# Optimization experiments

Measured on AMD Instinct MI355X. Metric: run time of the kernel, lower is better.

## Reference

```python
import jax, jax.numpy as jnp
import numpy as np
import math

H = 12  # config['n_heads']

def _ln(x, w, b, eps=1e-5):
    mu = x.mean(-1, keepdims=True)
    var = ((x - mu) ** 2).mean(-1, keepdims=True)
    return (x - mu) / jnp.sqrt(var + eps) * w + b

def setup_inputs() -> dict:
    key = jax.random.key(0)
    B, L, D, R = 2, 1024, 768, 128
    d_head = D // H
    ks = jax.random.split(key, 6)
    s = 0.02
    return {
        "x": jax.random.normal(ks[0], (B, L, D), jnp.float32),
        "Wqkv": jax.random.normal(ks[1], (D, 3 * D), jnp.float32) * s,
        "bqkv": jnp.zeros((3 * D,), jnp.float32),
        "Wb1": jax.random.normal(ks[2], (D, R), jnp.float32) * s,
        "Wb2": jax.random.normal(ks[3], (R, H * 5), jnp.float32) * s,
        "temperature": jnp.ones((1,), jnp.float32) * 0.5,
        "Wproj": jax.random.normal(ks[4], (D, D), jnp.float32) * s,
        "bproj": jnp.zeros((D,), jnp.float32),
        "ln_w": jnp.ones((D,), jnp.float32),
        "ln_b": jnp.zeros((D,), jnp.float32),
        "mn_w": jnp.ones((d_head,), jnp.float32),
        "mn_b": jnp.zeros((d_head,), jnp.float32),
    }

def reference(x, Wqkv, bqkv, Wb1, Wb2, temperature, Wproj, bproj, ln_w, ln_b, mn_w, mn_b):
    B, L, D = x.shape
    d = D // H
    x_norm = _ln(x, ln_w, ln_b)
    qkv = x_norm @ Wqkv + bqkv
    q, k, v = jnp.split(qkv, 3, axis=-1)
    # bottleneck gating operates on raw x (not x_norm), matching the source
    params = (jax.nn.silu(x @ Wb1) @ Wb2).reshape(B, L, H, 5)
    sem_amp = jax.nn.sigmoid(params[..., 0])
    sem_phase = jnp.tanh(params[..., 1]) * math.pi
    ctx_amp = jax.nn.sigmoid(params[..., 2])
    ctx_phase = jnp.tanh(params[..., 3]) * math.pi
    # decay_rate = 0.1 + 0.89*sigmoid(params[...,4]) is computed in the source
    # but never used in the final output path, so it is omitted here.
    temp = jnp.clip(temperature, 0.1, 2.0)  # shape (1,), broadcasts
    interference = jnp.tanh(sem_amp * ctx_amp * jnp.cos(sem_phase - ctx_phase)) * temp
    gate = jax.nn.sigmoid(interference)  # [B,L,H]
    q_f = (jax.nn.elu(q) + 1.0).reshape(B, L, H, d)
    k_f = (jax.nn.elu(k) + 1.0).reshape(B, L, H, d)
    v_f = v.reshape(B, L, H, d)
    # gated KV outer products and causal prefix-sum (linear attention state)
    kv_gated = jnp.einsum('blhd,blhe->blhde', k_f, v_f) * (1.0 + gate)[..., None, None]
    kv_states = jnp.cumsum(kv_gated, axis=1)       # [B,L,H,d,d]
    z_states = jnp.cumsum(k_f, axis=1)             # [B,L,H,d]
    out_num = jnp.einsum('blhd,blhde->blhe', q_f, kv_states)
    den = jnp.sum(q_f * z_states, axis=-1, keepdims=True) + 1e-6
    out = _ln(out_num / den, mn_w, mn_b)           # LayerNorm over d_head
    attn_out = out.reshape(B, L, D)
    return (attn_out @ Wproj + bproj, gate)
```

## Files before the change

kernel.cpp:

```cpp
#include <hip/hip_runtime.h>
#include <hip/hip_bf16.h>
#include <math.h>

constexpr int Bc = 2, Lc = 1024, Dc = 768, Hc = 12, dh = 64, Rc = 128;
constexpr int BL = Bc * Lc;
constexpr int TD = 3 * Dc;
constexpr int CH = 64;
constexpr int NC = Lc / CH;
constexpr int BH = Bc * Hc;

typedef __attribute__((ext_vector_type(8))) short bf16x8;
typedef __attribute__((ext_vector_type(4))) float f32x4;

__device__ __forceinline__ float bf2f(short u) {
    union { float f; unsigned int i; } c;
    c.i = ((unsigned int)(unsigned short)u) << 16;
    return c.f;
}
__device__ __forceinline__ short f2b(float f) {
    __hip_bfloat16 h = __float2bfloat16(f);
    return *reinterpret_cast<short*>(&h);
}

#define GLOAD_LDS16(gp, lp)                                                        \
    __builtin_amdgcn_global_load_lds(                                              \
        (const __attribute__((address_space(1))) void*)(gp),                       \
        (__attribute__((address_space(3))) void*)(lp), 16, 0, 0)

__device__ __forceinline__ void do_transpose(const float* __restrict__ W,
                                             __hip_bfloat16* __restrict__ WT,
                                             int K, int N, int bx, int by,
                                             int tid, float* t) {
    int k0 = by * 32, n0 = bx * 32;
    int r = tid >> 5, c = tid & 31;
#pragma unroll
    for (int i = 0; i < 4; i++)
        t[(r + i * 8) * 33 + c] = W[(size_t)(k0 + r + i * 8) * N + n0 + c];
    __syncthreads();
#pragma unroll
    for (int i = 0; i < 4; i++)
        WT[(size_t)(n0 + r + i * 8) * K + k0 + c] = __float2bfloat16(t[c * 33 + r + i * 8]);
}

constexpr int NT1 = (TD / 32) * (Dc / 32);
constexpr int NT2 = (Dc / 32) * (Dc / 32);
constexpr int NT3 = (Rc / 32) * (Dc / 32);
constexpr int NPREP = NT1 + NT2 + NT3 + BL;

__global__ __launch_bounds__(256)
void prep_kernel(const float* __restrict__ x, const float* __restrict__ ln_w,
                 const float* __restrict__ ln_b,
                 const float* __restrict__ Wqkv, const float* __restrict__ Wproj,
                 const float* __restrict__ Wb1,
                 __hip_bfloat16* __restrict__ xnb, __hip_bfloat16* __restrict__ xb,
                 __hip_bfloat16* __restrict__ WqkvT, __hip_bfloat16* __restrict__ WprojT,
                 __hip_bfloat16* __restrict__ Wb1T) {
    __shared__ float shm[32 * 33];
    int bid = blockIdx.x, tid = threadIdx.x;
    if (bid < NT1) { do_transpose(Wqkv, WqkvT, Dc, TD, bid % 72, bid / 72, tid, shm); return; }
    bid -= NT1;
    if (bid < NT2) { do_transpose(Wproj, WprojT, Dc, Dc, bid % 24, bid / 24, tid, shm); return; }
    bid -= NT2;
    if (bid < NT3) { do_transpose(Wb1, Wb1T, Dc, Rc, bid % 4, bid / 4, tid, shm); return; }
    bid -= NT3;
    int row = bid;
    const float* xr = x + (size_t)row * Dc;
    __hip_bfloat16* yr = xnb + (size_t)row * Dc;
    __hip_bfloat16* xbr = xb + (size_t)row * Dc;
    float v[3];
    float s = 0.f;
#pragma unroll
    for (int i = 0; i < 3; i++) { v[i] = xr[tid + i * 256]; s += v[i]; }
    shm[tid] = s; __syncthreads();
    for (int off = 128; off > 0; off >>= 1) {
        if (tid < off) shm[tid] += shm[tid + off];
        __syncthreads();
    }
    float mu = shm[0] / (float)Dc;
    __syncthreads();
    float s2 = 0.f;
#pragma unroll
    for (int i = 0; i < 3; i++) { float d = v[i] - mu; s2 += d * d; }
    shm[tid] = s2; __syncthreads();
    for (int off = 128; off > 0; off >>= 1) {
        if (tid < off) shm[tid] += shm[tid + off];
        __syncthreads();
    }
    float rstd = rsqrtf(shm[0] / (float)Dc + 1e-5f);
#pragma unroll
    for (int i = 0; i < 3; i++) {
        int c = tid + i * 256;
        yr[c] = __float2bfloat16((v[i] - mu) * rstd * ln_w[c] + ln_b[c]);
        xbr[c] = __float2bfloat16(v[i]);
    }
}

constexpr int NQB = (BL / 128) * (TD / 64);
constexpr int NFAT = NQB + (BL / 128) * 2;
__global__ __launch_bounds__(256)
void fat_gemm_kernel(const __hip_bfloat16* __restrict__ A1,
                     const __hip_bfloat16* __restrict__ B1,
                     const float* __restrict__ bias1,
                     __hip_bfloat16* __restrict__ C1,
                     const __hip_bfloat16* __restrict__ A2,
                     const __hip_bfloat16* __restrict__ B2,
                     float* __restrict__ C2) {
    __shared__ short lds[2][128 * 64 + 64 * 64];
    int bid = blockIdx.x;
    bid = (bid & 7) * (NFAT / 8) + (bid >> 3);
    bool isq = bid < NQB;
    int bx, by, N;
    const __hip_bfloat16 *A, *BT;
    if (isq) { bx = bid % 36; by = bid / 36; A = A1; BT = B1; N = TD; }
    else     { int b2 = bid - NQB; bx = b2 % 2; by = b2 / 2; A = A2; BT = B2; N = Rc; }
    const int K = Dc;

    int tid = threadIdx.x;
    int wave = tid >> 6, lane = tid & 63;
    int l16 = lane & 15, l4 = lane >> 4;
    int m0 = by * 128, n0 = bx * 64;

    int r_in = lane >> 3;
    int s_src = (lane & 7) ^ r_in;
    const __hip_bfloat16* gsrcA = A  + (size_t)(m0 + wave * 32 + r_in) * K + s_src * 8;
    const __hip_bfloat16* gsrcB = BT + (size_t)(n0 + wave * 16 + r_in) * K + s_src * 8;

    int wr = (wave >> 1) * 64, wc = (wave & 1) * 32;
    int xs = l16 & 7;

    f32x4 acc[4][2];
#pragma unroll
    for (int i = 0; i < 4; i++)
#pragma unroll
        for (int j = 0; j < 2; j++) acc[i][j] = f32x4{0.f, 0.f, 0.f, 0.f};

    auto stage = [&](int buf, int kt) {
        short* lbA = &lds[buf][(wave * 32) * 64];
        short* lbB = &lds[buf][128 * 64 + (wave * 16) * 64];
        const __hip_bfloat16* gA = gsrcA + kt * 64;
        const __hip_bfloat16* gB = gsrcB + kt * 64;
#pragma unroll
        for (int i = 0; i < 4; i++)
            GLOAD_LDS16(gA + (size_t)i * 8 * K, lbA + i * 8 * 64);
#pragma unroll
        for (int i = 0; i < 2; i++)
            GLOAD_LDS16(gB + (size_t)i * 8 * K, lbB + i * 8 * 64);
    };
    auto compute = [&](int buf) {
        const short* As = &lds[buf][0];
        const short* Bs = &lds[buf][128 * 64];
#pragma unroll
        for (int kk = 0; kk < 2; kk++) {
            bf16x8 af[4], bfr[2];
            int slot = (kk * 4 + l4) ^ xs;
#pragma unroll
            for (int f = 0; f < 4; f++)
                af[f] = *reinterpret_cast<const bf16x8*>(
                    &As[(wr + f * 16 + l16) * 64 + slot * 8]);
#pragma unroll
            for (int f = 0; f < 2; f++)
                bfr[f] = *reinterpret_cast<const bf16x8*>(
                    &Bs[(wc + f * 16 + l16) * 64 + slot * 8]);
#pragma unroll
            for (int i = 0; i < 4; i++)
#pragma unroll
                for (int j = 0; j < 2; j++)
                    acc[i][j] = __builtin_amdgcn_mfma_f32_16x16x32_bf16(
                        af[i], bfr[j], acc[i][j], 0, 0, 0);
        }
    };

    int NT = K / 64;
    int cur = 0;
    stage(0, 0);
    __syncthreads();
    for (int t = 0; t < NT; t++) {
        if (t + 1 < NT) stage(cur ^ 1, t + 1);
        compute(cur);
        if (t + 1 < NT) { __syncthreads(); cur ^= 1; }
    }

    int crow = l4 * 4;
#pragma unroll
    for (int i = 0; i < 4; i++) {
#pragma unroll
        for (int j = 0; j < 2; j++) {
            int col = n0 + wc + j * 16 + l16;
            float bb = isq ? bias1[col] : 0.f;
#pragma unroll
            for (int r = 0; r < 4; r++) {
                int rowm = m0 + wr + i * 16 + crow + r;
                float v = acc[i][j][r] + bb;
                if (isq) {
                    C1[(size_t)rowm * N + col] = __float2bfloat16(v);
                } else {
                    v = v / (1.f + expf(-v));
                    C2[(size_t)rowm * N + col] = v;
                }
            }
        }
    }
}

__global__ __launch_bounds__(256)
void gemm64_kernel(const __hip_bfloat16* __restrict__ A,
                   const __hip_bfloat16* __restrict__ BT,
                   const float* __restrict__ bias,
                   float* __restrict__ C, int M, int N, int K, int nbx) {
    __shared__ short lds[2][128 * 64];
    int nwg = gridDim.x;
    int bid = blockIdx.x;
    if ((nwg & 7) == 0) bid = (bid & 7) * (nwg >> 3) + (bid >> 3);
    int m0 = (bid / nbx) * 64, n0 = (bid % nbx) * 64;

    int tid = threadIdx.x;
    int wave = tid >> 6, lane = tid & 63;
    int l16 = lane & 15, l4 = lane >> 4;

    int r_in = lane >> 3;
    int s_src = (lane & 7) ^ r_in;
    const __hip_bfloat16* gsrc = (wave < 2)
        ? A  + (size_t)(m0 + wave * 32 + r_in) * K + s_src * 8
        : BT + (size_t)(n0 + (wave - 2) * 32 + r_in) * K + s_src * 8;

    int wr = (wave >> 1) * 32, wc = (wave & 1) * 32;
    int xs = l16 & 7;

    f32x4 acc[2][2];
#pragma unroll
    for (int i = 0; i < 2; i++)
#pragma unroll
        for (int j = 0; j < 2; j++) acc[i][j] = f32x4{0.f, 0.f, 0.f, 0.f};

    auto stage = [&](int buf, int kt) {
        const __hip_bfloat16* g = gsrc + kt * 64;
        short* lb = &lds[buf][wave * 32 * 64];
#pragma unroll
        for (int i = 0; i < 4; i++)
            GLOAD_LDS16(g + (size_t)i * 8 * K, lb + i * 8 * 64);
    };
    auto compute = [&](int buf) {
        const short* As = &lds[buf][0];
        const short* Bs = &lds[buf][64 * 64];
#pragma unroll
        for (int kk = 0; kk < 2; kk++) {
            bf16x8 af[2], bfr[2];
            int slot = (kk * 4 + l4) ^ xs;
#pragma unroll
            for (int f = 0; f < 2; f++) {
                af[f]  = *reinterpret_cast<const bf16x8*>(
                    &As[(wr + f * 16 + l16) * 64 + slot * 8]);
                bfr[f] = *reinterpret_cast<const bf16x8*>(
                    &Bs[(wc + f * 16 + l16) * 64 + slot * 8]);
            }
#pragma unroll
            for (int i = 0; i < 2; i++)
#pragma unroll
                for (int j = 0; j < 2; j++)
                    acc[i][j] = __builtin_amdgcn_mfma_f32_16x16x32_bf16(
                        af[i], bfr[j], acc[i][j], 0, 0, 0);
        }
    };

    int NT = K / 64;
    int cur = 0;
    stage(0, 0);
    __syncthreads();
    for (int t = 0; t < NT; t++) {
        if (t + 1 < NT) stage(cur ^ 1, t + 1);
        compute(cur);
        if (t + 1 < NT) { __syncthreads(); cur ^= 1; }
    }

    int crow = l4 * 4;
#pragma unroll
    for (int i = 0; i < 2; i++) {
#pragma unroll
        for (int j = 0; j < 2; j++) {
            int col = n0 + wc + j * 16 + l16;
            float bb = bias[col];
#pragma unroll
            for (int r = 0; r < 4; r++) {
                int rowm = m0 + wr + i * 16 + crow + r;
                C[(size_t)rowm * N + col] = acc[i][j][r] + bb;
            }
        }
    }
}

constexpr int LQ = 72;
__global__ __launch_bounds__(256)
void phaseA_kernel(const __hip_bfloat16* __restrict__ qkv, const float* __restrict__ tbuf,
                   const float* __restrict__ Wb2, const float* __restrict__ temperature,
                   float* __restrict__ gate_out,
                   float* __restrict__ SU, float* __restrict__ zc) {
    int bid = blockIdx.x;
    int bh = bid >> 4, c = bid & 15;
    int b = bh / Hc, h = bh % Hc;
    int tok0 = b * Lc + c * CH;
    __shared__ short KsT[64 * LQ];
    __shared__ short VT[80 * LQ];
    __shared__ float w2s[5 * 128];
    __shared__ float ogs[64];
    int tid = threadIdx.x;
    int wave = tid >> 6, lane = tid & 63;
    int l16 = lane & 15, l4 = lane >> 4;

    for (int i = tid; i < 640; i += 256) {
        int cc = i >> 7, r = i & 127;
        w2s[i] = Wb2[r * (Hc * 5) + h * 5 + cc];
    }
    bf16x8 k8[2], v8[2];
#pragma unroll
    for (int i = 0; i < 2; i++) {
        int c8 = tid + i * 256;
        int tt = c8 >> 3, d8 = (c8 & 7) * 8;
        size_t rowoff = (size_t)(tok0 + tt) * TD + h * dh;
        k8[i] = *reinterpret_cast<const bf16x8*>(qkv + rowoff + Dc + d8);
        v8[i] = *reinterpret_cast<const bf16x8*>(qkv + rowoff + 2 * Dc + d8);
    }
    for (int i = tid; i < 16 * LQ; i += 256) VT[64 * LQ + i] = 0;
    if (tid < 64) VT[64 * LQ + tid] = f2b(1.0f);
    __syncthreads();

    {
        int tt = tid >> 2, sub = tid & 3;
        const float* tr = tbuf + (size_t)(tok0 + tt) * Rc + sub * 32;
        float p[5] = {};
        for (int r4 = 0; r4 < 32; r4 += 4) {
            float4 tv = *reinterpret_cast<const float4*>(tr + r4);
#pragma unroll
            for (int cc = 0; cc < 5; cc++) {
                float4 w4 = *reinterpret_cast<const float4*>(&w2s[cc * 128 + sub * 32 + r4]);
                p[cc] = fmaf(tv.x, w4.x, fmaf(tv.y, w4.y,
                        fmaf(tv.z, w4.z, fmaf(tv.w, w4.w, p[cc]))));
            }
        }
#pragma unroll
        for (int cc = 0; cc < 5; cc++) {
            p[cc] += __shfl_xor(p[cc], 1, 64);
            p[cc] += __shfl_xor(p[cc], 2, 64);
        }
        if (sub == 0) {
            const float PI = 3.14159265358979323846f;
            float sem_amp = 1.f / (1.f + expf(-p[0]));
            float sem_phase = tanhf(p[1]) * PI;
            float ctx_amp = 1.f / (1.f + expf(-p[2]));
            float ctx_phase = tanhf(p[3]) * PI;
            float temp = fminf(fmaxf(temperature[0], 0.1f), 2.0f);
            float inter = tanhf(sem_amp * ctx_amp * cosf(sem_phase - ctx_phase)) * temp;
            float g = 1.f / (1.f + expf(-inter));
            gate_out[(size_t)(tok0 + tt) * Hc + h] = g;
            ogs[tt] = 1.f + g;
        }
    }
    __syncthreads();

#pragma unroll
    for (int i = 0; i < 2; i++) {
        int c8 = tid + i * 256;
        int tt = c8 >> 3, d8 = (c8 & 7) * 8;
        float gv = ogs[tt];
#pragma unroll
        for (int j = 0; j < 8; j++) {
            float kv = bf2f(k8[i][j]);
            KsT[(d8 + j) * LQ + tt] = f2b(kv > 0.f ? kv + 1.f : expf(kv));
            VT[(d8 + j) * LQ + tt]  = f2b(bf2f(v8[i][j]) * gv);
        }
    }
    __syncthreads();

    const short* arow = &KsT[(wave * 16 + l16) * LQ];
    f32x4 acc[5];
#pragma unroll
    for (int j = 0; j < 5; j++) acc[j] = f32x4{0.f, 0.f, 0.f, 0.f};
#pragma unroll
    for (int kk = 0; kk < 2; kk++) {
        bf16x8 af = *reinterpret_cast<const bf16x8*>(&arow[kk * 32 + l4 * 8]);
#pragma unroll
        for (int j = 0; j < 5; j++) {
            bf16x8 bfv = *reinterpret_cast<const bf16x8*>(
                &VT[(j * 16 + l16) * LQ + kk * 32 + l4 * 8]);
            acc[j] = __builtin_amdgcn_mfma_f32_16x16x32_bf16(af, bfv, acc[j], 0, 0, 0);
        }
    }
    int dbase = wave * 16 + l4 * 4;
    float* SUo = SU + (size_t)bid * 4096;
#pragma unroll
    for (int j = 0; j < 4; j++) {
        int e = j * 16 + l16;
#pragma unroll
        for (int r = 0; r < 4; r++)
            SUo[e * 64 + dbase + r] = acc[j][r];
    }
    if (l16 == 0) {
#pragma unroll
        for (int r = 0; r < 4; r++)
            zc[bid * 64 + dbase + r] = acc[4][r];
    }
}

__global__ __launch_bounds__(256)
void prefix_kernel(float* __restrict__ SU, float* __restrict__ zc) {
    int gid = blockIdx.x * 256 + threadIdx.x;
    if (gid < BH * 4096) {
        int bh = gid >> 12, i = gid & 4095;
        float* S = SU + (size_t)bh * NC * 4096 + i;
        float r[NC];
#pragma unroll
        for (int cc = 0; cc < NC; cc++) r[cc] = S[cc * 4096];
        float run = 0.f;
#pragma unroll
        for (int cc = 0; cc < NC; cc++) { float tv = r[cc]; S[cc * 4096] = run; run += tv; }
    } else {
        int g2 = gid - BH * 4096;
        if (g2 < BH * 64) {
            int bh = g2 >> 6, i = g2 & 63;
            float* z = zc + (size_t)bh * NC * 64 + i;
            float r[NC];
#pragma unroll
            for (int cc = 0; cc < NC; cc++) r[cc] = z[cc * 64];
            float run = 0.f;
#pragma unroll
            for (int cc = 0; cc < NC; cc++) { float tv = r[cc]; z[cc * 64] = run; run += tv; }
        }
    }
}

constexpr int LB = 136;
__global__ __launch_bounds__(256)
void phaseC_kernel(const __hip_bfloat16* __restrict__ qkv, const float* __restrict__ gate,
                   const float* __restrict__ SU, const float* __restrict__ zc,
                   const float* __restrict__ mn_w, const float* __restrict__ mn_b,
                   __hip_bfloat16* __restrict__ attn) {
    int bid = blockIdx.x;
    int bh = bid >> 4;
    int b = bh / Hc, h = bh % Hc;
    int tok0 = b * Lc + (bid & 15) * CH;
    __shared__ short Qs[64 * LQ];
    __shared__ short Ks[64 * LQ];
    __shared__ short Ps[64 * LQ];
    __shared__ short Bst[80 * LB];
    int tid = threadIdx.x;
    int wave = tid >> 6, lane = tid & 63;
    int l16 = lane & 15, l4 = lane >> 4;

    const float* SUp = SU + (size_t)bid * 4096;
    const float* zcp = zc + (size_t)bid * 64;

#pragma unroll
    for (int i = 0; i < 2; i++) {
        int c8 = tid + i * 256;
        int tt = c8 >> 3, d8 = (c8 & 7) * 8;
        size_t rowoff = (size_t)(tok0 + tt) * TD + h * dh;
        bf16x8 q8 = *reinterpret_cast<const bf16x8*>(qkv + rowoff + d8);
        bf16x8 k8 = *reinterpret_cast<const bf16x8*>(qkv + rowoff + Dc + d8);
        bf16x8 v8 = *reinterpret_cast<const bf16x8*>(qkv + rowoff + 2 * Dc + d8);
        float gv = 1.f + gate[(size_t)(tok0 + tt) * Hc + h];
        short qo[8], ko[8];
#pragma unroll
        for (int j = 0; j < 8; j++) {
            float qv = bf2f(q8[j]);
            qo[j] = f2b(qv > 0.f ? qv + 1.f : expf(qv));
            float kv = bf2f(k8[j]);
            ko[j] = f2b(kv > 0.f ? kv + 1.f : expf(kv));
            Bst[(d8 + j) * LB + tt] = f2b(bf2f(v8[j]) * gv);
        }
        *reinterpret_cast<bf16x8*>(&Qs[tt * LQ + d8]) = *reinterpret_cast<bf16x8*>(qo);
        *reinterpret_cast<bf16x8*>(&Ks[tt * LQ + d8]) = *reinterpret_cast<bf16x8*>(ko);
        float4 sa = *reinterpret_cast<const float4*>(SUp + tt * 64 + d8);
        float4 sb = *reinterpret_cast<const float4*>(SUp + tt * 64 + d8 + 4);
        short so[8] = { f2b(sa.x), f2b(sa.y), f2b(sa.z), f2b(sa.w),
                        f2b(sb.x), f2b(sb.y), f2b(sb.z), f2b(sb.w) };
        *reinterpret_cast<bf16x8*>(&Bst[tt * LB + 64 + d8]) = *reinterpret_cast<bf16x8*>(so);
    }
    if (tid < 64) {
        Bst[64 * LB + tid] = f2b(1.0f);
        Bst[64 * LB + 64 + tid] = f2b(zcp[tid]);
    } else {
        for (int i2 = tid - 64; i2 < 15 * LB; i2 += 192) Bst[65 * LB + i2] = 0;
    }
    __syncthreads();

    const short* arow = &Qs[(wave * 16 + l16) * LQ];
    f32x4 accp[4];
#pragma unroll
    for (int j = 0; j < 4; j++) accp[j] = f32x4{0.f, 0.f, 0.f, 0.f};
#pragma unroll
    for (int kk = 0; kk < 2; kk++) {
        bf16x8 af = *reinterpret_cast<const bf16x8*>(&arow[kk * 32 + l4 * 8]);
#pragma unroll
        for (int j = 0; j < 4; j++) {
            bf16x8 bfv = *reinterpret_cast<const bf16x8*>(
                &Ks[(j * 16 + l16) * LQ + kk * 32 + l4 * 8]);
            accp[j] = __builtin_amdgcn_mfma_f32_16x16x32_bf16(af, bfv, accp[j], 0, 0, 0);
        }
    }
#pragma unroll
    for (int j = 0; j < 4; j++) {
#pragma unroll
        for (int r = 0; r < 4; r++) {
            int l = wave * 16 + l4 * 4 + r;
            int t = j * 16 + l16;
            float pv = (t <= l) ? accp[j][r] : 0.f;
            Ps[l * LQ + t] = f2b(pv);
        }
    }
    __syncthreads();

    const short* prow = &Ps[(wave * 16 + l16) * LQ];
    f32x4 acc[5];
#pragma unroll
    for (int j = 0; j < 5; j++) acc[j] = f32x4{0.f, 0.f, 0.f, 0.f};
#pragma unroll
    for (int kk = 0; kk < 4; kk++) {
        bf16x8 af = (kk < 2)
            ? *reinterpret_cast<const bf16x8*>(&prow[kk * 32 + l4 * 8])
            : *reinterpret_cast<const bf16x8*>(&arow[(kk - 2) * 32 + l4 * 8]);
#pragma unroll
        for (int j = 0; j < 5; j++) {
            bf16x8 bfv = *reinterpret_cast<const bf16x8*>(
                &Bst[(j * 16 + l16) * LB + kk * 32 + l4 * 8]);
            acc[j] = __builtin_amdgcn_mfma_f32_16x16x32_bf16(af, bfv, acc[j], 0, 0, 0);
        }
    }

#pragma unroll
    for (int r = 0; r < 4; r++) {
        float den = __shfl(acc[4][r], l4 * 16) + 1e-6f;
        float inv = 1.f / den;
        float v0 = acc[0][r] * inv, v1 = acc[1][r] * inv;
        float v2 = acc[2][r] * inv, v3 = acc[3][r] * inv;
        float s1 = v0 + v1 + v2 + v3;
        float s2 = v0 * v0 + v1 * v1 + v2 * v2 + v3 * v3;
#pragma unroll
        for (int m = 1; m < 16; m <<= 1) {
            s1 += __shfl_xor(s1, m, 64);
            s2 += __shfl_xor(s2, m, 64);
        }
        float mu = s1 * (1.f / 64.f);
        float rstd = rsqrtf(s2 * (1.f / 64.f) - mu * mu + 1e-5f);
        int l = wave * 16 + l4 * 4 + r;
        __hip_bfloat16* orow = attn + (size_t)(tok0 + l) * Dc + h * dh;
        float vj[4] = {v0, v1, v2, v3};
#pragma unroll
        for (int j = 0; j < 4; j++) {
            int e = j * 16 + l16;
            orow[e] = __float2bfloat16((vj[j] - mu) * rstd * mn_w[e] + mn_b[e]);
        }
    }
}

extern "C" void kernel_launch(void* const* d_in, const int* in_sizes, int n_in,
                              void* d_out, int out_size, void* d_ws, size_t ws_size,
                              hipStream_t stream) {
    const float* x     = (const float*)d_in[0];
    const float* Wqkv  = (const float*)d_in[1];
    const float* bqkv  = (const float*)d_in[2];
    const float* Wb1   = (const float*)d_in[3];
    const float* Wb2   = (const float*)d_in[4];
    const float* temp  = (const float*)d_in[5];
    const float* Wproj = (const float*)d_in[6];
    const float* bproj = (const float*)d_in[7];
    const float* ln_w  = (const float*)d_in[8];
    const float* ln_b  = (const float*)d_in[9];
    const float* mn_w  = (const float*)d_in[10];
    const float* mn_b  = (const float*)d_in[11];

    float* out0 = (float*)d_out;
    float* gate = out0 + (size_t)BL * Dc;

    float* ws   = (float*)d_ws;
    float* tbuf = ws;
    float* SU   = tbuf + (size_t)BL * Rc;
    float* zc   = SU + (size_t)BH * NC * 4096;
    __hip_bfloat16* bfr = (__hip_bfloat16*)(zc + (size_t)BH * NC * 64);
    __hip_bfloat16* qkvb   = bfr;
    __hip_bfloat16* xnb    = qkvb + (size_t)BL * TD;
    __hip_bfloat16* xb     = xnb + (size_t)BL * Dc;
    __hip_bfloat16* attnb  = xb + (size_t)BL * Dc;
    __hip_bfloat16* WqkvT  = attnb + (size_t)BL * Dc;
    __hip_bfloat16* WprojT = WqkvT + (size_t)TD * Dc;
    __hip_bfloat16* Wb1T   = WprojT + (size_t)Dc * Dc;

    prep_kernel<<<NPREP, 256, 0, stream>>>(x, ln_w, ln_b, Wqkv, Wproj, Wb1,
                                           xnb, xb, WqkvT, WprojT, Wb1T);
    fat_gemm_kernel<<<NFAT, 256, 0, stream>>>(xnb, WqkvT, bqkv, qkvb, xb, Wb1T, tbuf);
    phaseA_kernel<<<BH * NC, 256, 0, stream>>>(qkvb, tbuf, Wb2, temp, gate, SU, zc);
    prefix_kernel<<<(BH * 4096 + BH * 64 + 255) / 256, 256, 0, stream>>>(SU, zc);
    phaseC_kernel<<<BH * NC, 256, 0, stream>>>(qkvb, gate, SU, zc, mn_w, mn_b, attnb);
    gemm64_kernel<<<(BL / 64) * (Dc / 64), 256, 0, stream>>>(
        attnb, WprojT, bproj, out0, BL, Dc, Dc, Dc / 64);
}
```

Before: 58.68 us.

## Fuse phaseA, prefix, phaseC and projection GEMM into persistent kernel with grid barriers

Merges the four post-QKV kernels into one launch of 384 blocks that synchronise through a software grid barrier built on atomics. Each block keeps its Q, K and gated V tiles in shared memory from phase A into phase C, so they are not reloaded from global memory. This removes three launch gaps and the tail idling between kernels. In exchange it adds the cost of the atomic spin barriers and a memset per call, and it depends on all 384 blocks being resident at once; launch bounds of 256 threads with 2 blocks per CU are set to allow that.

```diff
diff --git a/kernel.cpp b/kernel.cpp
--- a/kernel.cpp
+++ b/kernel.cpp
@@ -8,6 +8,7 @@
 constexpr int CH = 64;
 constexpr int NC = Lc / CH;
 constexpr int BH = Bc * Hc;
+constexpr int NMEGA = BH * NC;
 
 typedef __attribute__((ext_vector_type(8))) short bf16x8;
 typedef __attribute__((ext_vector_type(4))) float f32x4;
@@ -26,6 +27,26 @@
     __builtin_amdgcn_global_load_lds(                                              \
         (const __attribute__((address_space(1))) void*)(gp),                       \
         (__attribute__((address_space(3))) void*)(lp), 16, 0, 0)
+
+__device__ __forceinline__ void grid_barrier(unsigned* bar, int idx, unsigned nb) {
+    __syncthreads();
+    if (threadIdx.x == 0) {
+        unsigned* cnt   = bar + idx * 16;
+        unsigned* sense = bar + idx * 16 + 8;
+        __threadfence();
+        unsigned old = atomicAdd(sense, 0u);
+        if (atomicAdd(cnt, 1u) == nb - 1) {
+            atomicExch(cnt, 0u);
+            __threadfence();
+            atomicAdd(sense, 1u);
+        } else {
+            while (atomicAdd(sense, 0u) == old)
+                __builtin_amdgcn_s_sleep(8);
+        }
+        __threadfence();
+    }
+    __syncthreads();
+}
 
 __device__ __forceinline__ void do_transpose(const float* __restrict__ W,
                                              __hip_bfloat16* __restrict__ WT,
@@ -202,124 +223,48 @@
     }
 }
 
-__global__ __launch_bounds__(256)
-void gemm64_kernel(const __hip_bfloat16* __restrict__ A,
-                   const __hip_bfloat16* __restrict__ BT,
-                   const float* __restrict__ bias,
-                   float* __restrict__ C, int M, int N, int K, int nbx) {
-    __shared__ short lds[2][128 * 64];
-    int nwg = gridDim.x;
+constexpr int LQ = 72;
+__global__ __launch_bounds__(256, 2)
+void mega_kernel(const __hip_bfloat16* __restrict__ qkv, const float* __restrict__ tbuf,
+                 const float* __restrict__ Wb2, const float* __restrict__ temperature,
+                 float* __restrict__ gate_out, float* __restrict__ SU, float* __restrict__ zc,
+                 const float* __restrict__ mn_w, const float* __restrict__ mn_b,
+                 __hip_bfloat16* __restrict__ attn,
+                 const __hip_bfloat16* __restrict__ WprojT, const float* __restrict__ bproj,
+                 float* __restrict__ out0, unsigned* __restrict__ bar) {
+    alignas(16) __shared__ char pool[50688];
+    short* VT   = (short*)pool;
+    short* KsT  = (short*)(pool + 11520);
+    short* Qs   = (short*)(pool + 20736);
+    short* KsRM = (short*)(pool + 29952);
+    float* w2s  = (float*)(pool + 39168);
+    float* ogs  = (float*)(pool + 41728);
+    short* BstS = (short*)(pool + 39168);
+
     int bid = blockIdx.x;
-    if ((nwg & 7) == 0) bid = (bid & 7) * (nwg >> 3) + (bid >> 3);
-    int m0 = (bid / nbx) * 64, n0 = (bid % nbx) * 64;
-
     int tid = threadIdx.x;
     int wave = tid >> 6, lane = tid & 63;
     int l16 = lane & 15, l4 = lane >> 4;
 
-    int r_in = lane >> 3;
-    int s_src = (lane & 7) ^ r_in;
-    const __hip_bfloat16* gsrc = (wave < 2)
-        ? A  + (size_t)(m0 + wave * 32 + r_in) * K + s_src * 8
-        : BT + (size_t)(n0 + (wave - 2) * 32 + r_in) * K + s_src * 8;
-
-    int wr = (wave >> 1) * 32, wc = (wave & 1) * 32;
-    int xs = l16 & 7;
-
-    f32x4 acc[2][2];
-#pragma unroll
-    for (int i = 0; i < 2; i++)
-#pragma unroll
-        for (int j = 0; j < 2; j++) acc[i][j] = f32x4{0.f, 0.f, 0.f, 0.f};
-
-    auto stage = [&](int buf, int kt) {
-        const __hip_bfloat16* g = gsrc + kt * 64;
-        short* lb = &lds[buf][wave * 32 * 64];
-#pragma unroll
-        for (int i = 0; i < 4; i++)
-            GLOAD_LDS16(g + (size_t)i * 8 * K, lb + i * 8 * 64);
-    };
-    auto compute = [&](int buf) {
-        const short* As = &lds[buf][0];
-        const short* Bs = &lds[buf][64 * 64];
-#pragma unroll
-        for (int kk = 0; kk < 2; kk++) {
-            bf16x8 af[2], bfr[2];
-            int slot = (kk * 4 + l4) ^ xs;
-#pragma unroll
-            for (int f = 0; f < 2; f++) {
-                af[f]  = *reinterpret_cast<const bf16x8*>(
-                    &As[(wr + f * 16 + l16) * 64 + slot * 8]);
-                bfr[f] = *reinterpret_cast<const bf16x8*>(
-                    &Bs[(wc + f * 16 + l16) * 64 + slot * 8]);
-            }
-#pragma unroll
-            for (int i = 0; i < 2; i++)
-#pragma unroll
-                for (int j = 0; j < 2; j++)
-                    acc[i][j] = __builtin_amdgcn_mfma_f32_16x16x32_bf16(
-                        af[i], bfr[j], acc[i][j], 0, 0, 0);
-        }
-    };
-
-    int NT = K / 64;
-    int cur = 0;
-    stage(0, 0);
-    __syncthreads();
-    for (int t = 0; t < NT; t++) {
-        if (t + 1 < NT) stage(cur ^ 1, t + 1);
-        compute(cur);
-        if (t + 1 < NT) { __syncthreads(); cur ^= 1; }
-    }
-
-    int crow = l4 * 4;
-#pragma unroll
-    for (int i = 0; i < 2; i++) {
-#pragma unroll
-        for (int j = 0; j < 2; j++) {
-            int col = n0 + wc + j * 16 + l16;
-            float bb = bias[col];
-#pragma unroll
-            for (int r = 0; r < 4; r++) {
-                int rowm = m0 + wr + i * 16 + crow + r;
-                C[(size_t)rowm * N + col] = acc[i][j][r] + bb;
-            }
-        }
-    }
-}
-
-constexpr int LQ = 72;
-__global__ __launch_bounds__(256)
-void phaseA_kernel(const __hip_bfloat16* __restrict__ qkv, const float* __restrict__ tbuf,
-                   const float* __restrict__ Wb2, const float* __restrict__ temperature,
-                   float* __restrict__ gate_out,
-                   float* __restrict__ SU, float* __restrict__ zc) {
-    int bid = blockIdx.x;
     int bh = bid >> 4, c = bid & 15;
     int b = bh / Hc, h = bh % Hc;
     int tok0 = b * Lc + c * CH;
-    __shared__ short KsT[64 * LQ];
-    __shared__ short VT[80 * LQ];
-    __shared__ float w2s[5 * 128];
-    __shared__ float ogs[64];
-    int tid = threadIdx.x;
-    int wave = tid >> 6, lane = tid & 63;
-    int l16 = lane & 15, l4 = lane >> 4;
 
     for (int i = tid; i < 640; i += 256) {
         int cc = i >> 7, r = i & 127;
         w2s[i] = Wb2[r * (Hc * 5) + h * 5 + cc];
     }
-    bf16x8 k8[2], v8[2];
+    bf16x8 q8[2], k8[2], v8[2];
 #pragma unroll
     for (int i = 0; i < 2; i++) {
         int c8 = tid + i * 256;
         int tt = c8 >> 3, d8 = (c8 & 7) * 8;
         size_t rowoff = (size_t)(tok0 + tt) * TD + h * dh;
+        q8[i] = *reinterpret_cast<const bf16x8*>(qkv + rowoff + d8);
         k8[i] = *reinterpret_cast<const bf16x8*>(qkv + rowoff + Dc + d8);
         v8[i] = *reinterpret_cast<const bf16x8*>(qkv + rowoff + 2 * Dc + d8);
     }
-    for (int i = tid; i < 16 * LQ; i += 256) VT[64 * LQ + i] = 0;
+    for (int i = tid; i < 15 * LQ; i += 256) VT[65 * LQ + i] = 0;
     if (tid < 64) VT[64 * LQ + tid] = f2b(1.0f);
     __syncthreads();
 
@@ -361,192 +306,238 @@
         int c8 = tid + i * 256;
         int tt = c8 >> 3, d8 = (c8 & 7) * 8;
         float gv = ogs[tt];
+        short qo[8], ko[8];
 #pragma unroll
         for (int j = 0; j < 8; j++) {
+            float qv = bf2f(q8[i][j]);
+            qo[j] = f2b(qv > 0.f ? qv + 1.f : expf(qv));
             float kv = bf2f(k8[i][j]);
-            KsT[(d8 + j) * LQ + tt] = f2b(kv > 0.f ? kv + 1.f : expf(kv));
+            ko[j] = f2b(kv > 0.f ? kv + 1.f : expf(kv));
+            KsT[(d8 + j) * LQ + tt] = ko[j];
             VT[(d8 + j) * LQ + tt]  = f2b(bf2f(v8[i][j]) * gv);
         }
-    }
-    __syncthreads();
-
-    const short* arow = &KsT[(wave * 16 + l16) * LQ];
-    f32x4 acc[5];
-#pragma unroll
-    for (int j = 0; j < 5; j++) acc[j] = f32x4{0.f, 0.f, 0.f, 0.f};
-#pragma unroll
-    for (int kk = 0; kk < 2; kk++) {
-        bf16x8 af = *reinterpret_cast<const bf16x8*>(&arow[kk * 32 + l4 * 8]);
-#pragma unroll
-        for (int j = 0; j < 5; j++) {
-            bf16x8 bfv = *reinterpret_cast<const bf16x8*>(
-                &VT[(j * 16 + l16) * LQ + kk * 32 + l4 * 8]);
-            acc[j] = __builtin_amdgcn_mfma_f32_16x16x32_bf16(af, bfv, acc[j], 0, 0, 0);
-        }
-    }
-    int dbase = wave * 16 + l4 * 4;
-    float* SUo = SU + (size_t)bid * 4096;
-#pragma unroll
-    for (int j = 0; j < 4; j++) {
-        int e = j * 16 + l16;
-#pragma unroll
-        for (int r = 0; r < 4; r++)
-            SUo[e * 64 + dbase + r] = acc[j][r];
-    }
-    if (l16 == 0) {
-#pragma unroll
-        for (int r = 0; r < 4; r++)
-            zc[bid * 64 + dbase + r] = acc[4][r];
-    }
-}
-
-__global__ __launch_bounds__(256)
-void prefix_kernel(float* __restrict__ SU, float* __restrict__ zc) {
-    int gid = blockIdx.x * 256 + threadIdx.x;
-    if (gid < BH * 4096) {
-        int bh = gid >> 12, i = gid & 4095;
-        float* S = SU + (size_t)bh * NC * 4096 + i;
+        *reinterpret_cast<bf16x8*>(&Qs[tt * LQ + d8])   = *reinterpret_cast<bf16x8*>(qo);
+        *reinterpret_cast<bf16x8*>(&KsRM[tt * LQ + d8]) = *reinterpret_cast<bf16x8*>(ko);
+    }
+    __syncthreads();
+
+    {
+        const short* arow = &KsT[(wave * 16 + l16) * LQ];
+        f32x4 acc[5];
+#pragma unroll
+        for (int j = 0; j < 5; j++) acc[j] = f32x4{0.f, 0.f, 0.f, 0.f};
+#pragma unroll
+        for (int kk = 0; kk < 2; kk++) {
+            bf16x8 af = *reinterpret_cast<const bf16x8*>(&arow[kk * 32 + l4 * 8]);
+#pragma unroll
+            for (int j = 0; j < 5; j++) {
+                bf16x8 bfv = *reinterpret_cast<const bf16x8*>(
+                    &VT[(j * 16 + l16) * LQ + kk * 32 + l4 * 8]);
+                acc[j] = __builtin_amdgcn_mfma_f32_16x16x32_bf16(af, bfv, acc[j], 0, 0, 0);
+            }
+        }
+        int dbase = wave * 16 + l4 * 4;
+        float* SUo = SU + (size_t)bid * 4096;
+#pragma unroll
+        for (int j = 0; j < 4; j++) {
+            int e = j * 16 + l16;
+#pragma unroll
+            for (int r = 0; r < 4; r++)
+                SUo[e * 64 + dbase + r] = acc[j][r];
+        }
+        if (l16 == 0) {
+#pragma unroll
+            for (int r = 0; r < 4; r++)
+                zc[bid * 64 + dbase + r] = acc[4][r];
+        }
+    }
+    grid_barrier(bar, 0, NMEGA);
+
+    {
+        int gid = bid * 256 + tid;
+        int pbh = gid >> 12, i = gid & 4095;
+        float* S = SU + (size_t)pbh * NC * 4096 + i;
         float r[NC];
 #pragma unroll
         for (int cc = 0; cc < NC; cc++) r[cc] = S[cc * 4096];
         float run = 0.f;
 #pragma unroll
         for (int cc = 0; cc < NC; cc++) { float tv = r[cc]; S[cc * 4096] = run; run += tv; }
-    } else {
-        int g2 = gid - BH * 4096;
-        if (g2 < BH * 64) {
-            int bh = g2 >> 6, i = g2 & 63;
-            float* z = zc + (size_t)bh * NC * 64 + i;
-            float r[NC];
-#pragma unroll
-            for (int cc = 0; cc < NC; cc++) r[cc] = z[cc * 64];
-            float run = 0.f;
-#pragma unroll
-            for (int cc = 0; cc < NC; cc++) { float tv = r[cc]; z[cc * 64] = run; run += tv; }
-        }
-    }
-}
-
-constexpr int LB = 136;
-__global__ __launch_bounds__(256)
-void phaseC_kernel(const __hip_bfloat16* __restrict__ qkv, const float* __restrict__ gate,
-                   const float* __restrict__ SU, const float* __restrict__ zc,
-                   const float* __restrict__ mn_w, const float* __restrict__ mn_b,
-                   __hip_bfloat16* __restrict__ attn) {
-    int bid = blockIdx.x;
-    int bh = bid >> 4;
-    int b = bh / Hc, h = bh % Hc;
-    int tok0 = b * Lc + (bid & 15) * CH;
-    __shared__ short Qs[64 * LQ];
-    __shared__ short Ks[64 * LQ];
-    __shared__ short Ps[64 * LQ];
-    __shared__ short Bst[80 * LB];
-    int tid = threadIdx.x;
-    int wave = tid >> 6, lane = tid & 63;
-    int l16 = lane & 15, l4 = lane >> 4;
-
-    const float* SUp = SU + (size_t)bid * 4096;
-    const float* zcp = zc + (size_t)bid * 64;
-
-#pragma unroll
-    for (int i = 0; i < 2; i++) {
-        int c8 = tid + i * 256;
-        int tt = c8 >> 3, d8 = (c8 & 7) * 8;
-        size_t rowoff = (size_t)(tok0 + tt) * TD + h * dh;
-        bf16x8 q8 = *reinterpret_cast<const bf16x8*>(qkv + rowoff + d8);
-        bf16x8 k8 = *reinterpret_cast<const bf16x8*>(qkv + rowoff + Dc + d8);
-        bf16x8 v8 = *reinterpret_cast<const bf16x8*>(qkv + rowoff + 2 * Dc + d8);
-        float gv = 1.f + gate[(size_t)(tok0 + tt) * Hc + h];
-        short qo[8], ko[8];
-#pragma unroll
-        for (int j = 0; j < 8; j++) {
-            float qv = bf2f(q8[j]);
-            qo[j] = f2b(qv > 0.f ? qv + 1.f : expf(qv));
-            float kv = bf2f(k8[j]);
-            ko[j] = f2b(kv > 0.f ? kv + 1.f : expf(kv));
-            Bst[(d8 + j) * LB + tt] = f2b(bf2f(v8[j]) * gv);
-        }
-        *reinterpret_cast<bf16x8*>(&Qs[tt * LQ + d8]) = *reinterpret_cast<bf16x8*>(qo);
-        *reinterpret_cast<bf16x8*>(&Ks[tt * LQ + d8]) = *reinterpret_cast<bf16x8*>(ko);
-        float4 sa = *reinterpret_cast<const float4*>(SUp + tt * 64 + d8);
-        float4 sb = *reinterpret_cast<const float4*>(SUp + tt * 64 + d8 + 4);
-        short so[8] = { f2b(sa.x), f2b(sa.y), f2b(sa.z), f2b(sa.w),
-                        f2b(sb.x), f2b(sb.y), f2b(sb.z), f2b(sb.w) };
-        *reinterpret_cast<bf16x8*>(&Bst[tt * LB + 64 + d8]) = *reinterpret_cast<bf16x8*>(so);
-    }
-    if (tid < 64) {
-        Bst[64 * LB + tid] = f2b(1.0f);
-        Bst[64 * LB + 64 + tid] = f2b(zcp[tid]);
-    } else {
-        for (int i2 = tid - 64; i2 < 15 * LB; i2 += 192) Bst[65 * LB + i2] = 0;
-    }
-    __syncthreads();
-
-    const short* arow = &Qs[(wave * 16 + l16) * LQ];
-    f32x4 accp[4];
-#pragma unroll
-    for (int j = 0; j < 4; j++) accp[j] = f32x4{0.f, 0.f, 0.f, 0.f};
-#pragma unroll
-    for (int kk = 0; kk < 2; kk++) {
-        bf16x8 af = *reinterpret_cast<const bf16x8*>(&arow[kk * 32 + l4 * 8]);
+        if (gid < BH * 64) {
+            int zbh = gid >> 6, zi = gid & 63;
+            float* z = zc + (size_t)zbh * NC * 64 + zi;
+            float rz[NC];
+#pragma unroll
+            for (int cc = 0; cc < NC; cc++) rz[cc] = z[cc * 64];
+            float runz = 0.f;
+#pragma unroll
+            for (int cc = 0; cc < NC; cc++) { float tv = rz[cc]; z[cc * 64] = runz; runz += tv; }
+        }
+    }
+    grid_barrier(bar, 1, NMEGA);
+
+    {
+        const float* SUp = SU + (size_t)bid * 4096;
+        const float* zcp = zc + (size_t)bid * 64;
+#pragma unroll
+        for (int i = 0; i < 2; i++) {
+            int c8 = tid + i * 256;
+            int tt = c8 >> 3, d8 = (c8 & 7) * 8;
+            float4 sa = *reinterpret_cast<const float4*>(SUp + tt * 64 + d8);
+            float4 sb = *reinterpret_cast<const float4*>(SUp + tt * 64 + d8 + 4);
+            short so[8] = { f2b(sa.x), f2b(sa.y), f2b(sa.z), f2b(sa.w),
+                            f2b(sb.x), f2b(sb.y), f2b(sb.z), f2b(sb.w) };
+            *reinterpret_cast<bf16x8*>(&BstS[tt * LQ + d8]) = *reinterpret_cast<bf16x8*>(so);
+        }
+        if (tid < 64) BstS[64 * LQ + tid] = f2b(zcp[tid]);
+        for (int i = tid; i < 15 * LQ; i += 256) BstS[65 * LQ + i] = 0;
+
+        const short* qrow = &Qs[(wave * 16 + l16) * LQ];
+        short* Ps = KsT;
+        f32x4 accp[4];
+#pragma unroll
+        for (int j = 0; j < 4; j++) accp[j] = f32x4{0.f, 0.f, 0.f, 0.f};
+#pragma unroll
+        for (int kk = 0; kk < 2; kk++) {
+            bf16x8 af = *reinterpret_cast<const bf16x8*>(&qrow[kk * 32 + l4 * 8]);
+#pragma unroll
+            for (int j = 0; j < 4; j++) {
+                bf16x8 bfv = *reinterpret_cast<const bf16x8*>(
+                    &KsRM[(j * 16 + l16) * LQ + kk * 32 + l4 * 8]);
+                accp[j] = __builtin_amdgcn_mfma_f32_16x16x32_bf16(af, bfv, accp[j], 0, 0, 0);
+            }
+        }
 #pragma unroll
         for (int j = 0; j < 4; j++) {
-            bf16x8 bfv = *reinterpret_cast<const bf16x8*>(
-                &Ks[(j * 16 + l16) * LQ + kk * 32 + l4 * 8]);
-            accp[j] = __builtin_amdgcn_mfma_f32_16x16x32_bf16(af, bfv, accp[j], 0, 0, 0);
-        }
-    }
-#pragma unroll
-    for (int j = 0; j < 4; j++) {
+#pragma unroll
+            for (int r = 0; r < 4; r++) {
+                int l = wave * 16 + l4 * 4 + r;
+                int t = j * 16 + l16;
+                float pv = (t <= l) ? accp[j][r] : 0.f;
+                Ps[l * LQ + t] = f2b(pv);
+            }
+        }
+        __syncthreads();
+
+        const short* prow = &Ps[(wave * 16 + l16) * LQ];
+        f32x4 acc[5];
+#pragma unroll
+        for (int j = 0; j < 5; j++) acc[j] = f32x4{0.f, 0.f, 0.f, 0.f};
+#pragma unroll
+        for (int kk = 0; kk < 4; kk++) {
+            bf16x8 af = (kk < 2)
+                ? *reinterpret_cast<const bf16x8*>(&prow[kk * 32 + l4 * 8])
+                : *reinterpret_cast<const bf16x8*>(&qrow[(kk - 2) * 32 + l4 * 8]);
+#pragma unroll
+            for (int j = 0; j < 5; j++) {
+                const short* btile = (kk < 2)
+                    ? &VT[(j * 16 + l16) * LQ + kk * 32 + l4 * 8]
+                    : &BstS[(j * 16 + l16) * LQ + (kk - 2) * 32 + l4 * 8];
+                bf16x8 bfv = *reinterpret_cast<const bf16x8*>(btile);
+                acc[j] = __builtin_amdgcn_mfma_f32_16x16x32_bf16(af, bfv, acc[j], 0, 0, 0);
+            }
+        }
 #pragma unroll
         for (int r = 0; r < 4; r++) {
+            float den = __shfl(acc[4][r], l4 * 16) + 1e-6f;
+            float inv = 1.f / den;
+            float v0 = acc[0][r] * inv, v1 = acc[1][r] * inv;
+            float v2 = acc[2][r] * inv, v3 = acc[3][r] * inv;
+            float s1 = v0 + v1 + v2 + v3;
+            float s2 = v0 * v0 + v1 * v1 + v2 * v2 + v3 * v3;
+#pragma unroll
+            for (int m = 1; m < 16; m <<= 1) {
+                s1 += __shfl_xor(s1, m, 64);
+                s2 += __shfl_xor(s2, m, 64);
+            }
+            float mu = s1 * (1.f / 64.f);
+            float rstd = rsqrtf(s2 * (1.f / 64.f) - mu * mu + 1e-5f);
             int l = wave * 16 + l4 * 4 + r;
-            int t = j * 16 + l16;
-            float pv = (t <= l) ? accp[j][r] : 0.f;
-            Ps[l * LQ + t] = f2b(pv);
-        }
-    }
-    __syncthreads();
-
-    const short* prow = &Ps[(wave * 16 + l16) * LQ];
-    f32x4 acc[5];
-#pragma unroll
-    for (int j = 0; j < 5; j++) acc[j] = f32x4{0.f, 0.f, 0.f, 0.f};
-#pragma unroll
-    for (int kk = 0; kk < 4; kk++) {
-        bf16x8 af = (kk < 2)
-            ? *reinterpret_cast<const bf16x8*>(&prow[kk * 32 + l4 * 8])
-            : *reinterpret_cast<const bf16x8*>(&arow[(kk - 2) * 32 + l4 * 8]);
-#pragma unroll
-        for (int j = 0; j < 5; j++) {
-            bf16x8 bfv = *reinterpret_cast<const bf16x8*>(
-                &Bst[(j * 16 + l16) * LB + kk * 32 + l4 * 8]);
-            acc[j] = __builtin_amdgcn_mfma_f32_16x16x32_bf16(af, bfv, acc[j], 0, 0, 0);
-        }
-    }
-
-#pragma unroll
-    for (int r = 0; r < 4; r++) {
-        float den = __shfl(acc[4][r], l4 * 16) + 1e-6f;
-        float inv = 1.f / den;
-        float v0 = acc[0][r] * inv, v1 = acc[1][r] * inv;
-        float v2 = acc[2][r] * inv, v3 = acc[3][r] * inv;
-        float s1 = v0 + v1 + v2 + v3;
-        float s2 = v0 * v0 + v1 * v1 + v2 * v2 + v3 * v3;
-#pragma unroll
-        for (int m = 1; m < 16; m <<= 1) {
-            s1 += __shfl_xor(s1, m, 64);
-            s2 += __shfl_xor(s2, m, 64);
-        }
-        float mu = s1 * (1.f / 64.f);
-        float rstd = rsqrtf(s2 * (1.f / 64.f) - mu * mu + 1e-5f);
-        int l = wave * 16 + l4 * 4 + r;
-        __hip_bfloat16* orow = attn + (size_t)(tok0 + l) * Dc + h * dh;
-        float vj[4] = {v0, v1, v2, v3};
-#pragma unroll
-        for (int j = 0; j < 4; j++) {
-            int e = j * 16 + l16;
-            orow[e] = __float2bfloat16((vj[j] - mu) * rstd * mn_w[e] + mn_b[e]);
+            __hip_bfloat16* orow = attn + (size_t)(tok0 + l) * Dc + h * dh;
+            float vj[4] = {v0, v1, v2, v3};
+#pragma unroll
+            for (int j = 0; j < 4; j++) {
+                int e = j * 16 + l16;
+                orow[e] = __float2bfloat16((vj[j] - mu) * rstd * mn_w[e] + mn_b[e]);
+            }
+        }
+    }
+    grid_barrier(bar, 2, NMEGA);
+
+    {
+        short* plds = (short*)pool;
+        const int K = Dc, N = Dc, nbx = Dc / 64;
+        int pbid = (bid & 7) * 48 + (bid >> 3);
+        int m0 = (pbid / nbx) * 64, n0 = (pbid % nbx) * 64;
+
+        int r_in = lane >> 3;
+        int s_src = (lane & 7) ^ r_in;
+        const __hip_bfloat16* gsrc = (wave < 2)
+            ? attn   + (size_t)(m0 + wave * 32 + r_in) * K + s_src * 8
+            : WprojT + (size_t)(n0 + (wave - 2) * 32 + r_in) * K + s_src * 8;
+
+        int wr = (wave >> 1) * 32, wc = (wave & 1) * 32;
+        int xs = l16 & 7;
+
+        f32x4 acc[2][2];
+#pragma unroll
+        for (int i = 0; i < 2; i++)
+#pragma unroll
+            for (int j = 0; j < 2; j++) acc[i][j] = f32x4{0.f, 0.f, 0.f, 0.f};
+
+        auto stage = [&](int buf, int kt) {
+            const __hip_bfloat16* g = gsrc + kt * 64;
+            short* lb = plds + buf * 8192 + wave * 32 * 64;
+#pragma unroll
+            for (int i = 0; i < 4; i++)
+                GLOAD_LDS16(g + (size_t)i * 8 * K, lb + i * 8 * 64);
+        };
+        auto compute = [&](int buf) {
+            const short* As = plds + buf * 8192;
+            const short* Bs = plds + buf * 8192 + 64 * 64;
+#pragma unroll
+            for (int kk = 0; kk < 2; kk++) {
+                bf16x8 af[2], bfr[2];
+                int slot = (kk * 4 + l4) ^ xs;
+#pragma unroll
+                for (int f = 0; f < 2; f++) {
+                    af[f]  = *reinterpret_cast<const bf16x8*>(
+                        &As[(wr + f * 16 + l16) * 64 + slot * 8]);
+                    bfr[f] = *reinterpret_cast<const bf16x8*>(
+                        &Bs[(wc + f * 16 + l16) * 64 + slot * 8]);
+                }
+#pragma unroll
+                for (int i = 0; i < 2; i++)
+#pragma unroll
+                    for (int j = 0; j < 2; j++)
+                        acc[i][j] = __builtin_amdgcn_mfma_f32_16x16x32_bf16(
+                            af[i], bfr[j], acc[i][j], 0, 0, 0);
+            }
+        };
+
+        int NT = K / 64;
+        int cur = 0;
+        stage(0, 0);
+        __syncthreads();
+        for (int t = 0; t < NT; t++) {
+            if (t + 1 < NT) stage(cur ^ 1, t + 1);
+            compute(cur);
+            if (t + 1 < NT) { __syncthreads(); cur ^= 1; }
+        }
+
+        int crow = l4 * 4;
+#pragma unroll
+        for (int i = 0; i < 2; i++) {
+#pragma unroll
+            for (int j = 0; j < 2; j++) {
+                int col = n0 + wc + j * 16 + l16;
+                float bb = bproj[col];
+#pragma unroll
+                for (int r = 0; r < 4; r++) {
+                    int rowm = m0 + wr + i * 16 + crow + r;
+                    out0[(size_t)rowm * N + col] = acc[i][j][r] + bb;
+                }
+            }
         }
     }
 }
@@ -570,8 +561,8 @@
     float* out0 = (float*)d_out;
     float* gate = out0 + (size_t)BL * Dc;
 
-    float* ws   = (float*)d_ws;
-    float* tbuf = ws;
+    unsigned* bar = (unsigned*)d_ws;
+    float* tbuf = (float*)d_ws + 64;
     float* SU   = tbuf + (size_t)BL * Rc;
     float* zc   = SU + (size_t)BH * NC * 4096;
     __hip_bfloat16* bfr = (__hip_bfloat16*)(zc + (size_t)BH * NC * 64);
@@ -583,12 +574,10 @@
     __hip_bfloat16* WprojT = WqkvT + (size_t)TD * Dc;
     __hip_bfloat16* Wb1T   = WprojT + (size_t)Dc * Dc;
 
+    hipMemsetAsync(bar, 0, 256, stream);
     prep_kernel<<<NPREP, 256, 0, stream>>>(x, ln_w, ln_b, Wqkv, Wproj, Wb1,
                                            xnb, xb, WqkvT, WprojT, Wb1T);
     fat_gemm_kernel<<<NFAT, 256, 0, stream>>>(xnb, WqkvT, bqkv, qkvb, xb, Wb1T, tbuf);
-    phaseA_kernel<<<BH * NC, 256, 0, stream>>>(qkvb, tbuf, Wb2, temp, gate, SU, zc);
-    prefix_kernel<<<(BH * 4096 + BH * 64 + 255) / 256, 256, 0, stream>>>(SU, zc);
-    phaseC_kernel<<<BH * NC, 256, 0, stream>>>(qkvb, gate, SU, zc, mn_w, mn_b, attnb);
-    gemm64_kernel<<<(BL / 64) * (Dc / 64), 256, 0, stream>>>(
-        attnb, WprojT, bproj, out0, BL, Dc, Dc, Dc / 64);
-}
+    mega_kernel<<<NMEGA, 256, 0, stream>>>(qkvb, tbuf, Wb2, temp, gate, SU, zc,
+                                           mn_w, mn_b, attnb, WprojT, bproj, out0, bar);
+}
```

Result: slower. 175.6 us (+199.3%).

## Fuse chunk prefix scan into phaseA via last-block atomic counter

Applied to the files above, without the earlier changes.

Removes the separate prefix_kernel launch. Each phaseA block atomically bumps a per-(batch,head) counter, and the last chunk block to finish runs the exclusive prefix sum over all 16 chunk states for that head. A hipMemsetAsync resets the counters each call. This saves one kernel launch and its gap, but the scan now runs in only 24 blocks, serialized behind the tail of phaseA, and adds a memset.

```diff
diff --git a/kernel.cpp b/kernel.cpp
--- a/kernel.cpp
+++ b/kernel.cpp
@@ -293,7 +293,8 @@
 void phaseA_kernel(const __hip_bfloat16* __restrict__ qkv, const float* __restrict__ tbuf,
                    const float* __restrict__ Wb2, const float* __restrict__ temperature,
                    float* __restrict__ gate_out,
-                   float* __restrict__ SU, float* __restrict__ zc) {
+                   float* __restrict__ SU, float* __restrict__ zc,
+                   unsigned* __restrict__ cnt) {
     int bid = blockIdx.x;
     int bh = bid >> 4, c = bid & 15;
     int b = bh / Hc, h = bh % Hc;
@@ -302,6 +303,7 @@
     __shared__ short VT[80 * LQ];
     __shared__ float w2s[5 * 128];
     __shared__ float ogs[64];
+    __shared__ unsigned lastFlag;
     int tid = threadIdx.x;
     int wave = tid >> 6, lane = tid & 63;
     int l16 = lane & 15, l4 = lane >> 4;
@@ -398,31 +400,33 @@
         for (int r = 0; r < 4; r++)
             zc[bid * 64 + dbase + r] = acc[4][r];
     }
-}
-
-__global__ __launch_bounds__(256)
-void prefix_kernel(float* __restrict__ SU, float* __restrict__ zc) {
-    int gid = blockIdx.x * 256 + threadIdx.x;
-    if (gid < BH * 4096) {
-        int bh = gid >> 12, i = gid & 4095;
-        float* S = SU + (size_t)bh * NC * 4096 + i;
-        float r[NC];
-#pragma unroll
-        for (int cc = 0; cc < NC; cc++) r[cc] = S[cc * 4096];
-        float run = 0.f;
-#pragma unroll
-        for (int cc = 0; cc < NC; cc++) { float tv = r[cc]; S[cc * 4096] = run; run += tv; }
-    } else {
-        int g2 = gid - BH * 4096;
-        if (g2 < BH * 64) {
-            int bh = g2 >> 6, i = g2 & 63;
-            float* z = zc + (size_t)bh * NC * 64 + i;
+
+    __syncthreads();
+    if (tid == 0) {
+        __threadfence();
+        lastFlag = (atomicAdd(&cnt[bh], 1u) == NC - 1) ? 1u : 0u;
+    }
+    __syncthreads();
+    if (lastFlag == 0) return;
+    __threadfence();
+    {
+        float* S = SU + (size_t)bh * NC * 4096;
+        for (int i = tid; i < 4096; i += 256) {
+            float r[NC];
+#pragma unroll
+            for (int cc = 0; cc < NC; cc++) r[cc] = S[cc * 4096 + i];
+            float run = 0.f;
+#pragma unroll
+            for (int cc = 0; cc < NC; cc++) { S[cc * 4096 + i] = run; run += r[cc]; }
+        }
+        if (tid < 64) {
+            float* z = zc + (size_t)bh * NC * 64 + tid;
             float r[NC];
 #pragma unroll
             for (int cc = 0; cc < NC; cc++) r[cc] = z[cc * 64];
             float run = 0.f;
 #pragma unroll
-            for (int cc = 0; cc < NC; cc++) { float tv = r[cc]; z[cc * 64] = run; run += tv; }
+            for (int cc = 0; cc < NC; cc++) { z[cc * 64] = run; run += r[cc]; }
         }
     }
 }
@@ -570,8 +574,8 @@
     float* out0 = (float*)d_out;
     float* gate = out0 + (size_t)BL * Dc;
 
-    float* ws   = (float*)d_ws;
-    float* tbuf = ws;
+    unsigned* cnt = (unsigned*)d_ws;
+    float* tbuf = (float*)d_ws + 64;
     float* SU   = tbuf + (size_t)BL * Rc;
     float* zc   = SU + (size_t)BH * NC * 4096;
     __hip_bfloat16* bfr = (__hip_bfloat16*)(zc + (size_t)BH * NC * 64);
@@ -583,11 +587,11 @@
     __hip_bfloat16* WprojT = WqkvT + (size_t)TD * Dc;
     __hip_bfloat16* Wb1T   = WprojT + (size_t)Dc * Dc;
 
+    hipMemsetAsync(cnt, 0, 256, stream);
     prep_kernel<<<NPREP, 256, 0, stream>>>(x, ln_w, ln_b, Wqkv, Wproj, Wb1,
                                            xnb, xb, WqkvT, WprojT, Wb1T);
     fat_gemm_kernel<<<NFAT, 256, 0, stream>>>(xnb, WqkvT, bqkv, qkvb, xb, Wb1T, tbuf);
-    phaseA_kernel<<<BH * NC, 256, 0, stream>>>(qkvb, tbuf, Wb2, temp, gate, SU, zc);
-    prefix_kernel<<<(BH * 4096 + BH * 64 + 255) / 256, 256, 0, stream>>>(SU, zc);
+    phaseA_kernel<<<BH * NC, 256, 0, stream>>>(qkvb, tbuf, Wb2, temp, gate, SU, zc, cnt);
     phaseC_kernel<<<BH * NC, 256, 0, stream>>>(qkvb, gate, SU, zc, mn_w, mn_b, attnb);
     gemm64_kernel<<<(BL / 64) * (Dc / 64), 256, 0, stream>>>(
         attnb, WprojT, bproj, out0, BL, Dc, Dc, Dc / 64);
```

Result: slower. 103.1 us (+75.7%).
